# Performance work log

Measured on AMD Instinct MI355X. Metric: run time of the kernel, lower is better.

Reference implementation:

```python
import jax, jax.numpy as jnp
import numpy as np


def _make_P(states):
    # Matches HMMLayer.__init__: 0.99 self-transition, uniform remainder.
    P = np.ones((states, states), dtype=np.float32) * (0.01 / (states - 1))
    np.fill_diagonal(P, 0.99)
    return jnp.asarray(P)


def setup_inputs() -> dict:
    key = jax.random.key(0)
    B, T, K = 128, 1024, 256
    x = jax.random.normal(key, (B, T, K), dtype=jnp.float32)
    P = _make_P(K)
    p0 = jnp.full((K,), 1.0 / K, dtype=jnp.float32)  # uniform initial state dist
    return {"x": x, "P": P, "p0": p0}


def _forward_backward(y, P, p0):
    """Scaled HMM forward-backward.
    y  : (B, T, K) emission probabilities
    P  : (K, K) row-stochastic transition matrix
    p0 : (K,) initial state distribution
    Returns (posterior, alpha, beta), each (B, T, K).
    """
    B, T, K = y.shape
    yt = jnp.moveaxis(y, 1, 0)  # (T, B, K) for scan over time

    # --- forward (alpha) recursion with per-step normalization ---
    def fwd_step(alpha, y_t):
        a = (alpha @ P) * y_t                      # (B,K)@(K,K) -> (B,K)
        a = a / jnp.sum(a, axis=-1, keepdims=True)
        return a, a

    a0 = p0 * yt[0]
    a0 = a0 / jnp.sum(a0, axis=-1, keepdims=True)
    _, alphas = jax.lax.scan(fwd_step, a0, yt[1:])
    alpha = jnp.concatenate([a0[None], alphas], axis=0)  # (T,B,K)

    # --- backward (beta) recursion with per-step normalization ---
    def bwd_step(beta, y_next):
        # beta_t[i] = sum_j P[i,j] * y_{t+1}[j] * beta_{t+1}[j]
        b = (y_next * beta) @ P.T
        b = b / jnp.sum(b, axis=-1, keepdims=True)
        return b, b

    bT = jnp.ones((B, K), y.dtype)
    _, betas = jax.lax.scan(bwd_step, bT, yt[1:], reverse=True)
    beta = jnp.concatenate([betas, bT[None]], axis=0)  # (T,B,K)

    g = alpha * beta
    posterior = g / jnp.sum(g, axis=-1, keepdims=True)
    return (jnp.moveaxis(posterior, 0, 1),
            jnp.moveaxis(alpha, 0, 1),
            jnp.moveaxis(beta, 0, 1))


def reference(x, P, p0):
    # HMMLayer.call: sigmoid activation, then posterior from forward_backward
    # (training-phase branch, forward_backward(...)[0]).
    y = jax.nn.sigmoid(x)
    posterior, _, _ = _forward_backward(y, P, p0)
    return posterior
```

## Files before the change

### kernel.cpp

```cpp
#include <hip/hip_runtime.h>
#include <hip/hip_bf16.h>
#include <type_traits>


constexpr int BB = 128;
constexpr int TT = 1024;
constexpr int KK = 256;

template <int CTRL, int RM>
__device__ __forceinline__ float dpp_add(float v) {
  int t = __builtin_amdgcn_update_dpp(0, __float_as_int(v), CTRL, RM, 0xf, true);
  return v + __int_as_float(t);
}

__device__ __forceinline__ float wred_dpp(float v) {
  v = dpp_add<0x111, 0xf>(v);
  v = dpp_add<0x112, 0xf>(v);
  v = dpp_add<0x114, 0xf>(v);
  v = dpp_add<0x118, 0xf>(v);
  v = dpp_add<0x142, 0xa>(v);
  v = dpp_add<0x143, 0xc>(v);
  return __int_as_float(__builtin_amdgcn_readlane(__float_as_int(v), 63));
}

__device__ __forceinline__ float fsig(float x) {
  return __builtin_amdgcn_rcpf(1.0f + __expf(-x));
}

__device__ __forceinline__ unsigned short f2bf(float f) {
  unsigned int u = __float_as_uint(f);
  return (unsigned short)((u + 0x7FFFu + ((u >> 16) & 1u)) >> 16);
}
__device__ __forceinline__ float bf2f(unsigned short u) {
  return __uint_as_float((unsigned)u << 16);
}

__global__ __launch_bounds__(256) void sig_pass(const float* __restrict__ x,
                                                __hip_bfloat16* __restrict__ y) {
  const size_t i = (size_t)blockIdx.x * 256 + threadIdx.x;
  const float4 v = reinterpret_cast<const float4*>(x)[i];
  ushort4 o;
  o.x = f2bf(fsig(v.x));
  o.y = f2bf(fsig(v.y));
  o.z = f2bf(fsig(v.z));
  o.w = f2bf(fsig(v.w));
  reinterpret_cast<ushort4*>(y)[i] = o;
}

__device__ __forceinline__ float4 to_y(float4 v) {
  return make_float4(fsig(v.x), fsig(v.y), fsig(v.z), fsig(v.w));
}
__device__ __forceinline__ float4 to_y(ushort4 v) {
  return make_float4(bf2f(v.x), bf2f(v.y), bf2f(v.z), bf2f(v.w));
}

template <bool FUSED>
__global__ __launch_bounds__(64, 1) void hmm_recur(
    const void* __restrict__ src, const float* __restrict__ P,
    const float* __restrict__ p0,
    __hip_bfloat16* __restrict__ alpha, __hip_bfloat16* __restrict__ beta) {
  using VecT = typename std::conditional<FUSED, float4, ushort4>::type;
  const int seq = blockIdx.x;
  const int lane = threadIdx.x;
  const float diag = P[0];
  const float offd = P[1];
  const float cd = diag - offd;
  const float cod = offd;

  if (seq < BB) {
    const int b = seq;
    const VecT* srcv = reinterpret_cast<const VecT*>(src) + (size_t)b * TT * 64;
    ushort4* ar = reinterpret_cast<ushort4*>(alpha + (size_t)b * TT * KK);
    const float4 p0v = reinterpret_cast<const float4*>(p0)[lane];

    float v0 = 0.f, v1 = 0.f, v2 = 0.f, v3 = 0.f, S = 1.f;
    VecT bf0[8], bf1[8], bf2[8], bf3[8];

    auto loadF = [&](VecT* buf, int rbase) {
      if (rbase < TT) {
#pragma unroll
        for (int i = 0; i < 8; ++i) buf[i] = srcv[(size_t)(rbase + i) * 64 + lane];
      }
    };
    auto runF = [&](const VecT* buf, int tbase) {
#pragma unroll
      for (int i = 0; i < 8; ++i) {
        const int t = tbase + i;
        const float4 y = to_y(buf[i]);
        float w0, w1, w2, w3;
        if (t == 0) {
          w0 = p0v.x * y.x; w1 = p0v.y * y.y; w2 = p0v.z * y.z; w3 = p0v.w * y.w;
        } else {
          const float codS = cod * S;
          w0 = (codS + cd * v0) * y.x;
          w1 = (codS + cd * v1) * y.y;
          w2 = (codS + cd * v2) * y.z;
          w3 = (codS + cd * v3) * y.w;
        }
        S = wred_dpp((w0 + w1) + (w2 + w3));
        ushort4 pk;
        pk.x = f2bf(w0); pk.y = f2bf(w1); pk.z = f2bf(w2); pk.w = f2bf(w3);
        ar[t * 64 + lane] = pk;
        if ((t & 15) == 15) {
          const float r = __builtin_amdgcn_rcpf(S);
          w0 *= r; w1 *= r; w2 *= r; w3 *= r; S = 1.f;
        }
        v0 = w0; v1 = w1; v2 = w2; v3 = w3;
      }
    };

    loadF(bf0, 0); loadF(bf1, 8); loadF(bf2, 16);
    for (int tc = 0; tc < TT; tc += 32) {
      loadF(bf3, tc + 24); runF(bf0, tc);
      loadF(bf0, tc + 32); runF(bf1, tc + 8);
      loadF(bf1, tc + 40); runF(bf2, tc + 16);
      loadF(bf2, tc + 48); runF(bf3, tc + 24);
    }
  } else {
    const int b = seq - BB;
    const VecT* srcv = reinterpret_cast<const VecT*>(src) + (size_t)b * TT * 64;
    ushort4* br = reinterpret_cast<ushort4*>(beta + (size_t)b * TT * KK);

    float b0 = 1.f, b1 = 1.f, b2 = 1.f, b3 = 1.f;
    VecT bf0[8], bf1[8], bf2[8], bf3[8];

    auto loadB = [&](VecT* buf, int ubase) {
      if (ubase < TT) {
#pragma unroll
        for (int i = 0; i < 8; ++i) {
          const int u = ubase + i;
          const int row = (u == 0) ? (TT - 1) : (TT - u);
          buf[i] = srcv[(size_t)row * 64 + lane];
        }
      }
    };
    auto runB = [&](const VecT* buf, int ubase) {
#pragma unroll
      for (int i = 0; i < 8; ++i) {
        const int u = ubase + i;
        if (u == 0) {
          ushort4 pk;
          pk.x = pk.y = pk.z = pk.w = (unsigned short)0x3F80;
          br[(TT - 1) * 64 + lane] = pk;
          b0 = b1 = b2 = b3 = 1.f;
        } else {
          const float4 y = to_y(buf[i]);
          const float w0 = y.x * b0, w1 = y.y * b1, w2 = y.z * b2, w3 = y.w * b3;
          const float Sv = wred_dpp((w0 + w1) + (w2 + w3));
          const float codS = cod * Sv;
          b0 = codS + cd * w0;
          b1 = codS + cd * w1;
          b2 = codS + cd * w2;
          b3 = codS + cd * w3;
          ushort4 pk;
          pk.x = f2bf(b0); pk.y = f2bf(b1); pk.z = f2bf(b2); pk.w = f2bf(b3);
          br[(TT - 1 - u) * 64 + lane] = pk;
          if ((u & 15) == 15) {
            const float r = __builtin_amdgcn_rcpf(Sv);
            b0 *= r; b1 *= r; b2 *= r; b3 *= r;
          }
        }
      }
    };

    loadB(bf0, 0); loadB(bf1, 8); loadB(bf2, 16);
    for (int uc = 0; uc < TT; uc += 32) {
      loadB(bf3, uc + 24); runB(bf0, uc);
      loadB(bf0, uc + 32); runB(bf1, uc + 8);
      loadB(bf1, uc + 40); runB(bf2, uc + 16);
      loadB(bf2, uc + 48); runB(bf3, uc + 24);
    }
  }
}

__global__ __launch_bounds__(256) void hmm_post(
    const __hip_bfloat16* __restrict__ alpha,
    const __hip_bfloat16* __restrict__ beta, float* __restrict__ out) {
  const size_t gid = (size_t)blockIdx.x * 256 + threadIdx.x;
  const size_t row = gid >> 6;
  const int lane = (int)(gid & 63);
  const ushort4 av = reinterpret_cast<const ushort4*>(alpha)[row * 64 + lane];
  const ushort4 bv = reinterpret_cast<const ushort4*>(beta)[row * 64 + lane];
  const float g0 = bf2f(av.x) * bf2f(bv.x);
  const float g1 = bf2f(av.y) * bf2f(bv.y);
  const float g2 = bf2f(av.z) * bf2f(bv.z);
  const float g3 = bf2f(av.w) * bf2f(bv.w);
  const float s = wred_dpp((g0 + g1) + (g2 + g3));
  const float r = __builtin_amdgcn_rcpf(s);
  float4 o;
  o.x = g0 * r; o.y = g1 * r; o.z = g2 * r; o.w = g3 * r;
  reinterpret_cast<float4*>(out)[row * 64 + lane] = o;
}

extern "C" void kernel_launch(void* const* d_in, const int* in_sizes, int n_in,
                              void* d_out, int out_size, void* d_ws, size_t ws_size,
                              hipStream_t stream) {
  const float* x = (const float*)d_in[0];
  const float* P = (const float*)d_in[1];
  const float* p0 = (const float*)d_in[2];
  float* out = (float*)d_out;
  const size_t elems = (size_t)BB * TT * KK;

  __hip_bfloat16* alpha = (__hip_bfloat16*)d_ws;
  __hip_bfloat16* beta = alpha + elems;

  if (ws_size >= elems * 2 * 3) {
    __hip_bfloat16* y = beta + elems;
    sig_pass<<<(int)(elems / 4 / 256), 256, 0, stream>>>(x, y);
    hmm_recur<false><<<2 * BB, 64, 0, stream>>>((const void*)y, P, p0, alpha, beta);
  } else {
    hmm_recur<true><<<2 * BB, 64, 0, stream>>>((const void*)x, P, p0, alpha, beta);
  }
  hmm_post<<<(BB * TT) / 4, 256, 0, stream>>>(alpha, beta, out);
}
```

Measured before the change: 366.0 us.

## Precompute per-row emission sums to take reductions off the recurrence critical path

The sigmoid pre-pass now also writes C1[row] = offdiag * sum(y_row). The forward and backward recurrences use it to compute the next normalizer algebraically (S_next = cd*R + C1*S), so the wave reduction runs in parallel with the state update instead of between dependent steps. The change also switches to hardware v_cvt_pk_bf16 packing, uses a 16-deep register ring for prefetch, and stores the y/C1 scratch inside the output buffer. This removes the reduction from each step's serial dependency, at the cost of relying on the output buffer as scratch that hmm_post later overwrites.

```diff
diff --git a/kernel.cpp b/kernel.cpp
--- a/kernel.cpp
+++ b/kernel.cpp
@@ -1,11 +1,12 @@
 #include <hip/hip_runtime.h>
 #include <hip/hip_bf16.h>
-#include <type_traits>
 
 
 constexpr int BB = 128;
 constexpr int TT = 1024;
 constexpr int KK = 256;
+constexpr int PF = 16;
+constexpr size_t YPAD = 8192;
 
 template <int CTRL, int RM>
 __device__ __forceinline__ float dpp_add(float v) {
@@ -27,39 +28,35 @@
   return __builtin_amdgcn_rcpf(1.0f + __expf(-x));
 }
 
-__device__ __forceinline__ unsigned short f2bf(float f) {
-  unsigned int u = __float_as_uint(f);
-  return (unsigned short)((u + 0x7FFFu + ((u >> 16) & 1u)) >> 16);
-}
+__device__ __forceinline__ unsigned cvtpk_bf16(float lo, float hi) {
+  unsigned r;
+  asm("v_cvt_pk_bf16_f32 %0, %1, %2" : "=v"(r) : "v"(lo), "v"(hi));
+  return r;
+}
+__device__ __forceinline__ float lo16f(unsigned u) { return __uint_as_float(u << 16); }
+__device__ __forceinline__ float hi16f(unsigned u) { return __uint_as_float(u & 0xffff0000u); }
 __device__ __forceinline__ float bf2f(unsigned short u) {
   return __uint_as_float((unsigned)u << 16);
 }
 
-__global__ __launch_bounds__(256) void sig_pass(const float* __restrict__ x,
-                                                __hip_bfloat16* __restrict__ y) {
-  const size_t i = (size_t)blockIdx.x * 256 + threadIdx.x;
-  const float4 v = reinterpret_cast<const float4*>(x)[i];
-  ushort4 o;
-  o.x = f2bf(fsig(v.x));
-  o.y = f2bf(fsig(v.y));
-  o.z = f2bf(fsig(v.z));
-  o.w = f2bf(fsig(v.w));
-  reinterpret_cast<ushort4*>(y)[i] = o;
-}
-
-__device__ __forceinline__ float4 to_y(float4 v) {
-  return make_float4(fsig(v.x), fsig(v.y), fsig(v.z), fsig(v.w));
-}
-__device__ __forceinline__ float4 to_y(ushort4 v) {
-  return make_float4(bf2f(v.x), bf2f(v.y), bf2f(v.z), bf2f(v.w));
-}
-
-template <bool FUSED>
-__global__ __launch_bounds__(64, 1) void hmm_recur(
-    const void* __restrict__ src, const float* __restrict__ P,
-    const float* __restrict__ p0,
-    __hip_bfloat16* __restrict__ alpha, __hip_bfloat16* __restrict__ beta) {
-  using VecT = typename std::conditional<FUSED, float4, ushort4>::type;
+__global__ __launch_bounds__(256) void sig_pass2(const float* __restrict__ x,
+                                                 uint2* __restrict__ y,
+                                                 float* __restrict__ C1,
+                                                 const float* __restrict__ P) {
+  const int lane = threadIdx.x & 63;
+  const size_t row = ((size_t)blockIdx.x << 2) | (threadIdx.x >> 6);
+  const float4 v = reinterpret_cast<const float4*>(x)[row * 64 + lane];
+  const unsigned p01 = cvtpk_bf16(fsig(v.x), fsig(v.y));
+  const unsigned p23 = cvtpk_bf16(fsig(v.z), fsig(v.w));
+  y[row * 64 + lane] = make_uint2(p01, p23);
+  const float s = wred_dpp((lo16f(p01) + hi16f(p01)) + (lo16f(p23) + hi16f(p23)));
+  if (lane == 0) C1[row] = P[1] * s;
+}
+
+__global__ __launch_bounds__(64, 1) void hmm_recur2(
+    const uint2* __restrict__ y, const float* __restrict__ C1,
+    const float* __restrict__ P, const float* __restrict__ p0,
+    uint2* __restrict__ alpha, uint2* __restrict__ beta) {
   const int seq = blockIdx.x;
   const int lane = threadIdx.x;
   const float diag = P[0];
@@ -67,109 +64,124 @@
   const float cd = diag - offd;
   const float cod = offd;
 
+  uint2 ring[PF];
+
   if (seq < BB) {
     const int b = seq;
-    const VecT* srcv = reinterpret_cast<const VecT*>(src) + (size_t)b * TT * 64;
-    ushort4* ar = reinterpret_cast<ushort4*>(alpha + (size_t)b * TT * KK);
-    const float4 p0v = reinterpret_cast<const float4*>(p0)[lane];
-
-    float v0 = 0.f, v1 = 0.f, v2 = 0.f, v3 = 0.f, S = 1.f;
-    VecT bf0[8], bf1[8], bf2[8], bf3[8];
-
-    auto loadF = [&](VecT* buf, int rbase) {
-      if (rbase < TT) {
-#pragma unroll
-        for (int i = 0; i < 8; ++i) buf[i] = srcv[(size_t)(rbase + i) * 64 + lane];
+    const uint2* yb = y + (size_t)b * TT * 64;
+    uint2* ar = alpha + (size_t)b * TT * 64;
+    const float* c1b = C1 + (size_t)b * TT;
+
+    const uint2 yv0 = yb[lane];
+#pragma unroll
+    for (int i = 0; i < PF; ++i) ring[i] = yb[(size_t)(1 + i) * 64 + lane];
+
+    const float4 pv = reinterpret_cast<const float4*>(p0)[lane];
+    float v0 = pv.x * lo16f(yv0.x), v1 = pv.y * hi16f(yv0.x);
+    float v2 = pv.z * lo16f(yv0.y), v3 = pv.w * hi16f(yv0.y);
+    float S = wred_dpp((v0 + v1) + (v2 + v3));
+    ar[lane] = make_uint2(cvtpk_bf16(v0, v1), cvtpk_bf16(v2, v3));
+
+#define FSTEP(T_, SLOT_)                                                   \
+  {                                                                        \
+    const uint2 yv = ring[SLOT_];                                          \
+    ring[SLOT_] = yb[(size_t)((T_) + PF) * 64 + lane];                     \
+    const float y0 = lo16f(yv.x), y1 = hi16f(yv.x);                        \
+    const float y2 = lo16f(yv.y), y3 = hi16f(yv.y);                        \
+    const float R = wred_dpp((y0 * v0 + y1 * v1) + (y2 * v2 + y3 * v3));   \
+    const float Sn = cd * R + c1v * S;                                     \
+    const float sc = cod * S;                                              \
+    v0 = y0 * (cd * v0 + sc); v1 = y1 * (cd * v1 + sc);                    \
+    v2 = y2 * (cd * v2 + sc); v3 = y3 * (cd * v3 + sc);                    \
+    ar[(size_t)(T_) * 64 + lane] =                                         \
+        make_uint2(cvtpk_bf16(v0, v1), cvtpk_bf16(v2, v3));                \
+    S = Sn;                                                                \
+  }
+
+#pragma unroll
+    for (int i = 0; i < 15; ++i) {
+      const float c1v = c1b[i + 1];
+      FSTEP(i + 1, i);
+    }
+    {
+      const float rr = __builtin_amdgcn_rcpf(S);
+      v0 *= rr; v1 *= rr; v2 *= rr; v3 *= rr; S = 1.0f;
+    }
+
+#pragma unroll 1
+    for (int g = 1; g < 64; ++g) {
+      const int tb = g * 16;
+      float c1g[16];
+#pragma unroll
+      for (int j = 0; j < 16; ++j) c1g[j] = c1b[tb + j];
+#pragma unroll
+      for (int i = 0; i < 16; ++i) {
+        const int slot = (i + 15) & 15;
+        const float c1v = c1g[i];
+        FSTEP(tb + i, slot);
       }
-    };
-    auto runF = [&](const VecT* buf, int tbase) {
-#pragma unroll
-      for (int i = 0; i < 8; ++i) {
-        const int t = tbase + i;
-        const float4 y = to_y(buf[i]);
-        float w0, w1, w2, w3;
-        if (t == 0) {
-          w0 = p0v.x * y.x; w1 = p0v.y * y.y; w2 = p0v.z * y.z; w3 = p0v.w * y.w;
-        } else {
-          const float codS = cod * S;
-          w0 = (codS + cd * v0) * y.x;
-          w1 = (codS + cd * v1) * y.y;
-          w2 = (codS + cd * v2) * y.z;
-          w3 = (codS + cd * v3) * y.w;
-        }
-        S = wred_dpp((w0 + w1) + (w2 + w3));
-        ushort4 pk;
-        pk.x = f2bf(w0); pk.y = f2bf(w1); pk.z = f2bf(w2); pk.w = f2bf(w3);
-        ar[t * 64 + lane] = pk;
-        if ((t & 15) == 15) {
-          const float r = __builtin_amdgcn_rcpf(S);
-          w0 *= r; w1 *= r; w2 *= r; w3 *= r; S = 1.f;
-        }
-        v0 = w0; v1 = w1; v2 = w2; v3 = w3;
-      }
-    };
-
-    loadF(bf0, 0); loadF(bf1, 8); loadF(bf2, 16);
-    for (int tc = 0; tc < TT; tc += 32) {
-      loadF(bf3, tc + 24); runF(bf0, tc);
-      loadF(bf0, tc + 32); runF(bf1, tc + 8);
-      loadF(bf1, tc + 40); runF(bf2, tc + 16);
-      loadF(bf2, tc + 48); runF(bf3, tc + 24);
-    }
+      const float rr = __builtin_amdgcn_rcpf(S);
+      v0 *= rr; v1 *= rr; v2 *= rr; v3 *= rr; S = 1.0f;
+    }
+#undef FSTEP
   } else {
     const int b = seq - BB;
-    const VecT* srcv = reinterpret_cast<const VecT*>(src) + (size_t)b * TT * 64;
-    ushort4* br = reinterpret_cast<ushort4*>(beta + (size_t)b * TT * KK);
-
-    float b0 = 1.f, b1 = 1.f, b2 = 1.f, b3 = 1.f;
-    VecT bf0[8], bf1[8], bf2[8], bf3[8];
-
-    auto loadB = [&](VecT* buf, int ubase) {
-      if (ubase < TT) {
-#pragma unroll
-        for (int i = 0; i < 8; ++i) {
-          const int u = ubase + i;
-          const int row = (u == 0) ? (TT - 1) : (TT - u);
-          buf[i] = srcv[(size_t)row * 64 + lane];
-        }
+    const uint2* yb = y + (size_t)b * TT * 64;
+    uint2* br = beta + (size_t)b * TT * 64;
+    const float* c1b = C1 + (size_t)b * TT;
+
+    const uint2 yvL = yb[(size_t)(TT - 1) * 64 + lane];
+#pragma unroll
+    for (int i = 0; i < PF; ++i) ring[i] = yb[(size_t)(TT - 2 - i) * 64 + lane];
+
+    float m0 = lo16f(yvL.x), m1 = hi16f(yvL.x);
+    float m2 = lo16f(yvL.y), m3 = hi16f(yvL.y);
+    float S = wred_dpp((m0 + m1) + (m2 + m3));
+    br[(size_t)(TT - 1) * 64 + lane] = make_uint2(0x3F803F80u, 0x3F803F80u);
+
+#define BSTEP(T_, SLOT_)                                                   \
+  {                                                                        \
+    const uint2 yv = ring[SLOT_];                                          \
+    ring[SLOT_] = yb[(ptrdiff_t)((T_)-PF) * 64 + lane];                    \
+    const float y0 = lo16f(yv.x), y1 = hi16f(yv.x);                        \
+    const float y2 = lo16f(yv.y), y3 = hi16f(yv.y);                        \
+    const float R = wred_dpp((y0 * m0 + y1 * m1) + (y2 * m2 + y3 * m3));   \
+    const float Sn = cd * R + c1v * S;                                     \
+    const float sc = cod * S;                                              \
+    const float h0 = cd * m0 + sc, h1 = cd * m1 + sc;                      \
+    const float h2 = cd * m2 + sc, h3 = cd * m3 + sc;                      \
+    br[(size_t)(T_) * 64 + lane] =                                         \
+        make_uint2(cvtpk_bf16(h0, h1), cvtpk_bf16(h2, h3));                \
+    m0 = y0 * h0; m1 = y1 * h1; m2 = y2 * h2; m3 = y3 * h3;                \
+    S = Sn;                                                                \
+  }
+
+#pragma unroll
+    for (int k = 0; k < 15; ++k) {
+      const float c1v = c1b[1022 - k];
+      BSTEP(1022 - k, k);
+    }
+    {
+      const float rr = __builtin_amdgcn_rcpf(S);
+      m0 *= rr; m1 *= rr; m2 *= rr; m3 *= rr; S = 1.0f;
+    }
+
+#pragma unroll 1
+    for (int g = 1; g < 64; ++g) {
+      const int tb = 1007 - 16 * (g - 1);
+      float c1g[16];
+#pragma unroll
+      for (int j = 0; j < 16; ++j) c1g[j] = c1b[tb - 15 + j];
+#pragma unroll
+      for (int i = 0; i < 16; ++i) {
+        const int slot = (i + 15) & 15;
+        const float c1v = c1g[15 - i];
+        BSTEP(tb - i, slot);
       }
-    };
-    auto runB = [&](const VecT* buf, int ubase) {
-#pragma unroll
-      for (int i = 0; i < 8; ++i) {
-        const int u = ubase + i;
-        if (u == 0) {
-          ushort4 pk;
-          pk.x = pk.y = pk.z = pk.w = (unsigned short)0x3F80;
-          br[(TT - 1) * 64 + lane] = pk;
-          b0 = b1 = b2 = b3 = 1.f;
-        } else {
-          const float4 y = to_y(buf[i]);
-          const float w0 = y.x * b0, w1 = y.y * b1, w2 = y.z * b2, w3 = y.w * b3;
-          const float Sv = wred_dpp((w0 + w1) + (w2 + w3));
-          const float codS = cod * Sv;
-          b0 = codS + cd * w0;
-          b1 = codS + cd * w1;
-          b2 = codS + cd * w2;
-          b3 = codS + cd * w3;
-          ushort4 pk;
-          pk.x = f2bf(b0); pk.y = f2bf(b1); pk.z = f2bf(b2); pk.w = f2bf(b3);
-          br[(TT - 1 - u) * 64 + lane] = pk;
-          if ((u & 15) == 15) {
-            const float r = __builtin_amdgcn_rcpf(Sv);
-            b0 *= r; b1 *= r; b2 *= r; b3 *= r;
-          }
-        }
-      }
-    };
-
-    loadB(bf0, 0); loadB(bf1, 8); loadB(bf2, 16);
-    for (int uc = 0; uc < TT; uc += 32) {
-      loadB(bf3, uc + 24); runB(bf0, uc);
-      loadB(bf0, uc + 32); runB(bf1, uc + 8);
-      loadB(bf1, uc + 40); runB(bf2, uc + 16);
-      loadB(bf2, uc + 48); runB(bf3, uc + 24);
-    }
+      const float rr = __builtin_amdgcn_rcpf(S);
+      m0 *= rr; m1 *= rr; m2 *= rr; m3 *= rr; S = 1.0f;
+    }
+#undef BSTEP
   }
 }
 
@@ -195,21 +207,20 @@
 extern "C" void kernel_launch(void* const* d_in, const int* in_sizes, int n_in,
                               void* d_out, int out_size, void* d_ws, size_t ws_size,
                               hipStream_t stream) {
+  (void)in_sizes; (void)n_in; (void)out_size; (void)ws_size;
   const float* x = (const float*)d_in[0];
   const float* P = (const float*)d_in[1];
   const float* p0 = (const float*)d_in[2];
   float* out = (float*)d_out;
   const size_t elems = (size_t)BB * TT * KK;
 
-  __hip_bfloat16* alpha = (__hip_bfloat16*)d_ws;
-  __hip_bfloat16* beta = alpha + elems;
-
-  if (ws_size >= elems * 2 * 3) {
-    __hip_bfloat16* y = beta + elems;
-    sig_pass<<<(int)(elems / 4 / 256), 256, 0, stream>>>(x, y);
-    hmm_recur<false><<<2 * BB, 64, 0, stream>>>((const void*)y, P, p0, alpha, beta);
-  } else {
-    hmm_recur<true><<<2 * BB, 64, 0, stream>>>((const void*)x, P, p0, alpha, beta);
-  }
-  hmm_post<<<(BB * TT) / 4, 256, 0, stream>>>(alpha, beta, out);
-}
+  uint2* alpha = (uint2*)d_ws;
+  uint2* beta = alpha + elems / 4;
+  uint2* y = (uint2*)((char*)d_out + YPAD);
+  float* C1 = (float*)((char*)d_out + YPAD + elems * 2);
+
+  sig_pass2<<<(int)(BB * TT / 4), 256, 0, stream>>>(x, y, C1, P);
+  hmm_recur2<<<2 * BB, 64, 0, stream>>>(y, C1, P, p0, alpha, beta);
+  hmm_post<<<(BB * TT) / 4, 256, 0, stream>>>(
+      (const __hip_bfloat16*)alpha, (const __hip_bfloat16*)beta, out);
+}
```

Result: no change. 360.2 us (-1.6%).
